# Optimization experiments

Hardware: AMD Instinct MI355X
Metric: run time of the kernel (lower is better)

The kernel has to match this reference:

```python
import jax, jax.numpy as jnp
import numpy as np

SEQ_LEN, BATCH = 200, 4096
VOCAB, EMB_DIM, HID = 50000, 100, 300


def setup_inputs() -> dict:
    key = jax.random.key(0)
    ks = jax.random.split(key, 8)
    s = 0.05  # small init scale to keep tanh unsaturated
    return {
        "x": jax.random.randint(ks[0], (SEQ_LEN, BATCH), 0, VOCAB, dtype=jnp.int64 if jax.config.jax_enable_x64 else jnp.int32),
        "emb": jax.random.normal(ks[1], (VOCAB, EMB_DIM), jnp.float32) * s,
        "W_ih": jax.random.normal(ks[2], (HID, EMB_DIM), jnp.float32) * s,
        "b_ih": jnp.zeros((HID,), jnp.float32),
        "W_hh": jax.random.normal(ks[3], (HID, HID), jnp.float32) * s,
        "b_hh": jnp.zeros((HID,), jnp.float32),
        "W1": jax.random.normal(ks[4], (256, HID), jnp.float32) * s,
        "b1": jnp.zeros((256,), jnp.float32),
        "W2": jax.random.normal(ks[5], (2, 256), jnp.float32) * s,
        "b2": jnp.zeros((2,), jnp.float32),
    }


def reference(x, emb, W_ih, b_ih, W_hh, b_hh, W1, b1, W2, b2):
    # Embedding lookup: [T, B] -> [T, B, E]
    xe = emb[x]
    # Precompute input projections for all timesteps in one big GEMM: [T, B, H]
    xw = jnp.einsum('tbe,he->tbh', xe, W_ih) + b_ih + b_hh
    h0 = jnp.zeros((x.shape[1], W_hh.shape[0]), emb.dtype)

    def step(h, xw_t):
        h = jnp.tanh(xw_t + h @ W_hh.T)  # RNNCell: tanh(x Wih^T + bih + h Whh^T + bhh)
        return h, None

    h, _ = jax.lax.scan(step, h0, xw)
    h = jax.nn.relu(h @ W1.T + b1)
    return h @ W2.T + b2  # [B, 2]
```

## Files before the change

kernel.cpp:

```cpp
#include <hip/hip_runtime.h>

#define SEQ   200
#define BATCH 4096
#define EMB   100
#define HID   300
#define NH1   256
#define BM    16
#define NFRAG 13
#define FRB   14
#define FB    1024
#define BUFB  (FRB * FB)
#define NTMAX 3
#define NHF   10
#define H1P   260
#define PD    10

typedef _Float16 half8 __attribute__((ext_vector_type(8)));
typedef _Float16 half4h __attribute__((ext_vector_type(4)));
typedef float floatx4 __attribute__((ext_vector_type(4)));

__device__ __forceinline__ float fast_tanh(float x) {
    float e = __expf(2.0f * x);
    float r = __builtin_amdgcn_rcpf(e + 1.0f);
    return 1.0f - 2.0f * r;
}

__device__ __forceinline__ int fragoff(int m, int k) {
    return (k >> 5) * FB + ((k >> 3) & 3) * 256 + m * 16 + (k & 7) * 2;
}

#define T_LOOP(NTT)                                                                   \
    _Pragma("unroll 2")                                                               \
    for (int t = 0; t < SEQ; ++t) {                                                   \
        const int p = t & 1;                                                          \
        const char* rb = ub + p * BUFB + rdo;                                         \
        char*       wb = ub + (1 - p) * BUFB;                                         \
        half8 af[NFRAG];                                                              \
        _Pragma("unroll")                                                             \
        for (int kk = 0; kk < PD; ++kk) af[kk] = *(const half8*)(rb + kk * FB);       \
        if (is_st && (t + 1 < SEQ)) {                                                 \
            half4h hv; hv[0] = (_Float16)pf.x; hv[1] = (_Float16)pf.y;                \
                       hv[2] = (_Float16)pf.z; hv[3] = (_Float16)pf.w;                \
            *(half4h*)(wb + xwo) = hv;                                                \
        }                                                                             \
        if (is_st && (t + 2 < SEQ)) {                                                 \
            const int idx = xs[(t + 2) * BM + gr];                                    \
            pf = ((const float4*)emb)[idx * 25 + gc];                                 \
        }                                                                             \
        floatx4 acc[NTT];                                                             \
        _Pragma("unroll")                                                             \
        for (int kk = 0; kk < NFRAG; ++kk) {                                          \
            if (kk + PD < NFRAG) af[kk + PD] = *(const half8*)(rb + (kk + PD) * FB);  \
            _Pragma("unroll")                                                         \
            for (int tt = 0; tt < NTT; ++tt)                                          \
                acc[tt] = __builtin_amdgcn_mfma_f32_16x16x32_f16(                     \
                    Wb[tt][kk], af[kk], (kk == 0) ? biasv[tt] : acc[tt], 0, 0, 0);    \
        }                                                                             \
        _Pragma("unroll")                                                             \
        for (int tt = 0; tt < NTT; ++tt) {                                            \
            half4h hv;                                                                \
            _Pragma("unroll")                                                         \
            for (int r = 0; r < 4; ++r) hv[r] = (_Float16)fast_tanh(acc[tt][r]);      \
            *(half4h*)(wb + hwo[tt]) = hv;                                            \
        }                                                                             \
        asm volatile("s_waitcnt lgkmcnt(0)" ::: "memory");                            \
        __builtin_amdgcn_s_barrier();                                                 \
    }

__global__ void __launch_bounds__(512)
rnn_fused(const int* __restrict__ x, const float* __restrict__ emb,
          const float* __restrict__ W_ih, const float* __restrict__ b_ih,
          const float* __restrict__ W_hh, const float* __restrict__ b_hh,
          const float* __restrict__ W1, const float* __restrict__ b1,
          const float* __restrict__ W2, const float* __restrict__ b2,
          float* __restrict__ out)
{
    __shared__ __align__(16) _Float16 uf[2][FRB][512];
    __shared__ int   xs[SEQ * BM];
    __shared__ float h1s[BM][H1P];

    const int tid  = threadIdx.x;
    const int lane = tid & 63;
    const int w    = tid >> 6;
    const int ln15 = lane & 15;
    const int q    = lane >> 4;
    const int row0 = blockIdx.x * BM;

    const int t0 = (w < 3) ? 3 * w : 2 * w + 3;

    for (int i = tid; i < 2 * FRB * 512 / 2; i += 512) ((unsigned int*)uf)[i] = 0u;
    for (int i = tid; i < SEQ * BM; i += 512)
        xs[i] = x[(size_t)(i >> 4) * BATCH + row0 + (i & 15)];

    half8   Wb[NTMAX][NFRAG];
    floatx4 biasv[NTMAX];
#pragma unroll
    for (int tt = 0; tt < NTMAX; ++tt) {
        const int nb = (t0 + tt) * 16;
#pragma unroll
        for (int r = 0; r < 4; ++r) {
            const int col = nb + 4 * q + r;
            biasv[tt][r] = (col < HID) ? (b_ih[col] + b_hh[col]) : 0.0f;
        }
        const int n = nb + ln15;
#pragma unroll
        for (int kk = 0; kk < NFRAG; ++kk) {
            union { half8 h; unsigned int d[4]; } cv;
#pragma unroll
            for (int j = 0; j < 8; ++j) {
                const int k = kk * 32 + q * 8 + j;
                float v = 0.0f;
                if (n < HID) {
                    if (k < EMB)                        v = W_ih[n * EMB + k];
                    else if (k >= 112 && k < 112 + HID) v = W_hh[n * HID + (k - 112)];
                }
                cv.h[j] = (_Float16)v;
            }
            asm volatile("" : "+v"(cv.d[0]), "+v"(cv.d[1]), "+v"(cv.d[2]), "+v"(cv.d[3]));
            Wb[tt][kk] = cv.h;
        }
    }

    char* ub = (char*)uf;
    const int rdo = lane * 16;
    int hwo[NTMAX];
#pragma unroll
    for (int tt = 0; tt < NTMAX; ++tt)
        hwo[tt] = fragoff(ln15, 112 + (t0 + tt) * 16 + 4 * q);

    const bool is_st = (tid < 400);
    const int  gr = tid / 25, gc = tid - gr * 25;
    const int  xwo = fragoff(gr & 15, gc * 4);
    __syncthreads();

    float4 pf = {0.0f, 0.0f, 0.0f, 0.0f};
    if (is_st) {
        const int idx = xs[gr];
        const float4 f = ((const float4*)emb)[idx * 25 + gc];
        half4h hv; hv[0] = (_Float16)f.x; hv[1] = (_Float16)f.y;
                   hv[2] = (_Float16)f.z; hv[3] = (_Float16)f.w;
        *(half4h*)(ub + xwo) = hv;
        const int idx1 = xs[BM + gr];
        pf = ((const float4*)emb)[idx1 * 25 + gc];
    }
    __syncthreads();

    if (w < 3) {
        T_LOOP(3)
    } else {
        T_LOOP(2)
    }

    {
        const int hro = fragoff(ln15, 112 + q * 8);
        floatx4 hacc[2];
        int ncol[2];
#pragma unroll
        for (int tt = 0; tt < 2; ++tt) {
            const int n = (w * 2 + tt) * 16 + ln15;
            ncol[tt] = n;
            const float b = b1[n];
            hacc[tt][0] = b; hacc[tt][1] = b; hacc[tt][2] = b; hacc[tt][3] = b;
        }
#pragma unroll
        for (int kk = 0; kk < NHF; ++kk) {
            const half8 a = *(const half8*)(ub + hro + kk * FB);
#pragma unroll
            for (int tt = 0; tt < 2; ++tt) {
                half8 bv;
#pragma unroll
                for (int j = 0; j < 8; ++j) {
                    const int k = kk * 32 + q * 8 + j;
                    bv[j] = (_Float16)((k < HID) ? W1[ncol[tt] * HID + k] : 0.0f);
                }
                hacc[tt] = __builtin_amdgcn_mfma_f32_16x16x32_f16(bv, a, hacc[tt], 0, 0, 0);
            }
        }
#pragma unroll
        for (int tt = 0; tt < 2; ++tt) {
            float4 fv;
            fv.x = fmaxf(hacc[tt][0], 0.0f); fv.y = fmaxf(hacc[tt][1], 0.0f);
            fv.z = fmaxf(hacc[tt][2], 0.0f); fv.w = fmaxf(hacc[tt][3], 0.0f);
            *(float4*)&h1s[ln15][(w * 2 + tt) * 16 + 4 * q] = fv;
        }
    }
    __syncthreads();

    if (tid < 32) {
        const int r = tid & 15, o = tid >> 4;
        float a = b2[o];
        const float* ww = W2 + (size_t)o * NH1;
        for (int k = 0; k < NH1; ++k) a += h1s[r][k] * ww[k];
        out[(size_t)(row0 + r) * 2 + o] = a;
    }
}

extern "C" void kernel_launch(void* const* d_in, const int* in_sizes, int n_in,
                              void* d_out, int out_size, void* d_ws, size_t ws_size,
                              hipStream_t stream) {
    const int*   x    = (const int*)d_in[0];
    const float* emb  = (const float*)d_in[1];
    const float* W_ih = (const float*)d_in[2];
    const float* b_ih = (const float*)d_in[3];
    const float* W_hh = (const float*)d_in[4];
    const float* b_hh = (const float*)d_in[5];
    const float* W1   = (const float*)d_in[6];
    const float* b1   = (const float*)d_in[7];
    const float* W2   = (const float*)d_in[8];
    const float* b2   = (const float*)d_in[9];
    float* outp = (float*)d_out;

    hipLaunchKernelGGL(rnn_fused, dim3(BATCH / BM), dim3(512), 0, stream,
                       x, emb, W_ih, b_ih, W_hh, b_hh, W1, b1, W2, b2, outp);
}
```

Before: 326.5 us.

## Halve block to four waves with five output tiles each and redistribute gathers

Shrinks each RNN block from eight waves to four. Each wave now owns five 16-column output tiles of the hidden state (up from two or three), and the embedding-gather work is spread across threads so that some threads load up to three chunks. The aim is to cut per-step barrier cost and the number of waves that must synchronise, and to remove the 3/2 tile imbalance. In exchange, each wave holds more register-resident weight fragments (65 half8), so register pressure and spilling are a risk, and each wave has less latency-hiding parallelism per step.

New measurement: 417.3 us. 1.28x slower.

```diff
diff --git a/kernel.cpp b/kernel.cpp
--- a/kernel.cpp
+++ b/kernel.cpp
@@ -10,10 +10,11 @@
 #define FRB   14
 #define FB    1024
 #define BUFB  (FRB * FB)
-#define NTMAX 3
+#define NTMAX 5
 #define NHF   10
 #define H1P   260
-#define PD    10
+#define PD    7
+#define NCK   3
 
 typedef _Float16 half8 __attribute__((ext_vector_type(8)));
 typedef _Float16 half4h __attribute__((ext_vector_type(4)));
@@ -38,14 +39,20 @@
         half8 af[NFRAG];                                                              \
         _Pragma("unroll")                                                             \
         for (int kk = 0; kk < PD; ++kk) af[kk] = *(const half8*)(rb + kk * FB);       \
-        if (is_st && (t + 1 < SEQ)) {                                                 \
-            half4h hv; hv[0] = (_Float16)pf.x; hv[1] = (_Float16)pf.y;                \
-                       hv[2] = (_Float16)pf.z; hv[3] = (_Float16)pf.w;                \
-            *(half4h*)(wb + xwo) = hv;                                                \
-        }                                                                             \
-        if (is_st && (t + 2 < SEQ)) {                                                 \
-            const int idx = xs[(t + 2) * BM + gr];                                    \
-            pf = ((const float4*)emb)[idx * 25 + gc];                                 \
+        if (t + 1 < SEQ) {                                                            \
+            _Pragma("unroll")                                                         \
+            for (int j = 0; j < NCK; ++j) if (j < nck) {                              \
+                half4h hv; hv[0] = (_Float16)pf[j].x; hv[1] = (_Float16)pf[j].y;      \
+                           hv[2] = (_Float16)pf[j].z; hv[3] = (_Float16)pf[j].w;      \
+                *(half4h*)(wb + xwo[j]) = hv;                                         \
+            }                                                                         \
+        }                                                                             \
+        if (t + 2 < SEQ) {                                                            \
+            _Pragma("unroll")                                                         \
+            for (int j = 0; j < NCK; ++j) if (j < nck) {                              \
+                const int idx = xs[(t + 2) * BM + cgr[j]];                            \
+                pf[j] = ((const float4*)emb)[idx * 25 + cgc[j]];                      \
+            }                                                                         \
         }                                                                             \
         floatx4 acc[NTT];                                                             \
         _Pragma("unroll")                                                             \
@@ -67,7 +74,7 @@
         __builtin_amdgcn_s_barrier();                                                 \
     }
 
-__global__ void __launch_bounds__(512)
+__global__ void __launch_bounds__(256, 1)
 rnn_fused(const int* __restrict__ x, const float* __restrict__ emb,
           const float* __restrict__ W_ih, const float* __restrict__ b_ih,
           const float* __restrict__ W_hh, const float* __restrict__ b_hh,
@@ -86,10 +93,10 @@
     const int q    = lane >> 4;
     const int row0 = blockIdx.x * BM;
 
-    const int t0 = (w < 3) ? 3 * w : 2 * w + 3;
-
-    for (int i = tid; i < 2 * FRB * 512 / 2; i += 512) ((unsigned int*)uf)[i] = 0u;
-    for (int i = tid; i < SEQ * BM; i += 512)
+    const int t0 = 5 * w;
+
+    for (int i = tid; i < 2 * FRB * 512 / 2; i += 256) ((unsigned int*)uf)[i] = 0u;
+    for (int i = tid; i < SEQ * BM; i += 256)
         xs[i] = x[(size_t)(i >> 4) * BATCH + row0 + (i & 15)];
 
     half8   Wb[NTMAX][NFRAG];
@@ -128,36 +135,43 @@
     for (int tt = 0; tt < NTMAX; ++tt)
         hwo[tt] = fragoff(ln15, 112 + (t0 + tt) * 16 + 4 * q);
 
-    const bool is_st = (tid < 400);
-    const int  gr = tid / 25, gc = tid - gr * 25;
-    const int  xwo = fragoff(gr & 15, gc * 4);
+    int nck = 1;
+    int ckid[NCK]; ckid[0] = tid; ckid[1] = 0; ckid[2] = 0;
+    if (tid >= 192)      { ckid[1] = 256 + 2 * (tid - 192); ckid[2] = ckid[1] + 1; nck = 3; }
+    else if (tid >= 176) { ckid[1] = 384 + (tid - 176); nck = 2; }
+    int cgr[NCK], cgc[NCK], xwo[NCK];
+#pragma unroll
+    for (int j = 0; j < NCK; ++j) {
+        const int c = ckid[j];
+        cgr[j] = c / 25; cgc[j] = c - 25 * cgr[j];
+        xwo[j] = fragoff(cgr[j] & 15, cgc[j] * 4);
+    }
     __syncthreads();
 
-    float4 pf = {0.0f, 0.0f, 0.0f, 0.0f};
-    if (is_st) {
-        const int idx = xs[gr];
-        const float4 f = ((const float4*)emb)[idx * 25 + gc];
+    float4 pf[NCK];
+#pragma unroll
+    for (int j = 0; j < NCK; ++j) { pf[j].x = pf[j].y = pf[j].z = pf[j].w = 0.0f; }
+#pragma unroll
+    for (int j = 0; j < NCK; ++j) if (j < nck) {
+        const int idx = xs[cgr[j]];
+        const float4 f = ((const float4*)emb)[idx * 25 + cgc[j]];
         half4h hv; hv[0] = (_Float16)f.x; hv[1] = (_Float16)f.y;
                    hv[2] = (_Float16)f.z; hv[3] = (_Float16)f.w;
-        *(half4h*)(ub + xwo) = hv;
-        const int idx1 = xs[BM + gr];
-        pf = ((const float4*)emb)[idx1 * 25 + gc];
+        *(half4h*)(ub + xwo[j]) = hv;
+        const int idx1 = xs[BM + cgr[j]];
+        pf[j] = ((const float4*)emb)[idx1 * 25 + cgc[j]];
     }
     __syncthreads();
 
-    if (w < 3) {
-        T_LOOP(3)
-    } else {
-        T_LOOP(2)
-    }
+    T_LOOP(5)
 
     {
         const int hro = fragoff(ln15, 112 + q * 8);
-        floatx4 hacc[2];
-        int ncol[2];
-#pragma unroll
-        for (int tt = 0; tt < 2; ++tt) {
-            const int n = (w * 2 + tt) * 16 + ln15;
+        floatx4 hacc[4];
+        int ncol[4];
+#pragma unroll
+        for (int tt = 0; tt < 4; ++tt) {
+            const int n = (w * 4 + tt) * 16 + ln15;
             ncol[tt] = n;
             const float b = b1[n];
             hacc[tt][0] = b; hacc[tt][1] = b; hacc[tt][2] = b; hacc[tt][3] = b;
@@ -166,7 +180,7 @@
         for (int kk = 0; kk < NHF; ++kk) {
             const half8 a = *(const half8*)(ub + hro + kk * FB);
 #pragma unroll
-            for (int tt = 0; tt < 2; ++tt) {
+            for (int tt = 0; tt < 4; ++tt) {
                 half8 bv;
 #pragma unroll
                 for (int j = 0; j < 8; ++j) {
@@ -177,11 +191,11 @@
             }
         }
 #pragma unroll
-        for (int tt = 0; tt < 2; ++tt) {
+        for (int tt = 0; tt < 4; ++tt) {
             float4 fv;
             fv.x = fmaxf(hacc[tt][0], 0.0f); fv.y = fmaxf(hacc[tt][1], 0.0f);
             fv.z = fmaxf(hacc[tt][2], 0.0f); fv.w = fmaxf(hacc[tt][3], 0.0f);
-            *(float4*)&h1s[ln15][(w * 2 + tt) * 16 + 4 * q] = fv;
+            *(float4*)&h1s[ln15][(w * 4 + tt) * 16 + 4 * q] = fv;
         }
     }
     __syncthreads();
@@ -210,6 +224,6 @@
     const float* b2   = (const float*)d_in[9];
     float* outp = (float*)d_out;
 
-    hipLaunchKernelGGL(rnn_fused, dim3(BATCH / BM), dim3(512), 0, stream,
+    hipLaunchKernelGGL(rnn_fused, dim3(BATCH / BM), dim3(256), 0, stream,
                        x, emb, W_ih, b_ih, W_hh, b_hh, W1, b1, W2, b2, outp);
 }
```

## Split input and hidden projections, precompute next step's input MFMA off critical path

Applied to the files above, without the earlier changes.

Separates the fused [x|h] operand buffer into a double-buffered hidden buffer and a triple-buffered embedding buffer. The input projection for step t+1 (4 K-fragments) is now computed after the tanh of step t, so only the 10 hidden-state fragments sit on the serial recurrence path instead of 13. The embedding prefetch distance is extended by one step, and the store-thread mapping is changed to a simpler tid&15 / tid>>4 layout. This adds extra accumulator registers (accn) and LDS, and uses more VGPRs alongside the register-resident weights, which may raise spill or occupancy pressure.

New measurement: 431.9 us. 1.32x slower.

```diff
diff --git a/kernel.cpp b/kernel.cpp
--- a/kernel.cpp
+++ b/kernel.cpp
@@ -6,14 +6,14 @@
 #define HID   300
 #define NH1   256
 #define BM    16
-#define NFRAG 13
-#define FRB   14
+#define NHFR  10
+#define NXFR  4
 #define FB    1024
-#define BUFB  (FRB * FB)
+#define HBUF  (NHFR * FB)
+#define XBUF  (NXFR * FB)
 #define NTMAX 3
 #define NHF   10
 #define H1P   260
-#define PD    10
 
 typedef _Float16 half8 __attribute__((ext_vector_type(8)));
 typedef _Float16 half4h __attribute__((ext_vector_type(4)));
@@ -33,36 +33,55 @@
     _Pragma("unroll 2")                                                               \
     for (int t = 0; t < SEQ; ++t) {                                                   \
         const int p = t & 1;                                                          \
-        const char* rb = ub + p * BUFB + rdo;                                         \
-        char*       wb = ub + (1 - p) * BUFB;                                         \
-        half8 af[NFRAG];                                                              \
-        _Pragma("unroll")                                                             \
-        for (int kk = 0; kk < PD; ++kk) af[kk] = *(const half8*)(rb + kk * FB);       \
-        if (is_st && (t + 1 < SEQ)) {                                                 \
+        const char* rbh = ubh + p * HBUF + rdo;                                       \
+        char*       wbh = ubh + (1 - p) * HBUF;                                       \
+        half8 afh[NHFR];                                                              \
+        _Pragma("unroll")                                                             \
+        for (int kk = 0; kk < NHFR; ++kk) afh[kk] = *(const half8*)(rbh + kk * FB);   \
+        if (is_st && (t + 2 < SEQ)) {                                                 \
             half4h hv; hv[0] = (_Float16)pf.x; hv[1] = (_Float16)pf.y;                \
                        hv[2] = (_Float16)pf.z; hv[3] = (_Float16)pf.w;                \
-            *(half4h*)(wb + xwo) = hv;                                                \
-        }                                                                             \
-        if (is_st && (t + 2 < SEQ)) {                                                 \
-            const int idx = xs[(t + 2) * BM + gr];                                    \
+            *(half4h*)(ubx + sw + xwo) = hv;                                          \
+        }                                                                             \
+        if (is_st && (t + 3 < SEQ)) {                                                 \
+            const int idx = xs[(t + 3) * BM + gr];                                    \
             pf = ((const float4*)emb)[idx * 25 + gc];                                 \
         }                                                                             \
         floatx4 acc[NTT];                                                             \
         _Pragma("unroll")                                                             \
-        for (int kk = 0; kk < NFRAG; ++kk) {                                          \
-            if (kk + PD < NFRAG) af[kk + PD] = *(const half8*)(rb + (kk + PD) * FB);  \
+        for (int tt = 0; tt < NTT; ++tt) acc[tt] = accn[tt];                          \
+        _Pragma("unroll")                                                             \
+        for (int kk = 0; kk < NHFR; ++kk) {                                           \
             _Pragma("unroll")                                                         \
             for (int tt = 0; tt < NTT; ++tt)                                          \
-                acc[tt] = __builtin_amdgcn_mfma_f32_16x16x32_f16(                     \
-                    Wb[tt][kk], af[kk], (kk == 0) ? biasv[tt] : acc[tt], 0, 0, 0);    \
+                acc[tt] = __builtin_amdgcn_mfma_f32_16x16x32_f16(Wh[tt][kk], afh[kk], \
+                                                                 acc[tt], 0, 0, 0);   \
+        }                                                                             \
+        half8 afx[NXFR];                                                              \
+        if (t + 1 < SEQ) {                                                            \
+            _Pragma("unroll")                                                         \
+            for (int kk = 0; kk < NXFR; ++kk)                                         \
+                afx[kk] = *(const half8*)(ubx + sr + rdo + kk * FB);                  \
         }                                                                             \
         _Pragma("unroll")                                                             \
         for (int tt = 0; tt < NTT; ++tt) {                                            \
             half4h hv;                                                                \
             _Pragma("unroll")                                                         \
             for (int r = 0; r < 4; ++r) hv[r] = (_Float16)fast_tanh(acc[tt][r]);      \
-            *(half4h*)(wb + hwo[tt]) = hv;                                            \
-        }                                                                             \
+            *(half4h*)(wbh + hwo[tt]) = hv;                                           \
+        }                                                                             \
+        if (t + 1 < SEQ) {                                                            \
+            _Pragma("unroll")                                                         \
+            for (int tt = 0; tt < NTT; ++tt) {                                        \
+                accn[tt] = biasv[tt];                                                 \
+                _Pragma("unroll")                                                     \
+                for (int kk = 0; kk < NXFR; ++kk)                                     \
+                    accn[tt] = __builtin_amdgcn_mfma_f32_16x16x32_f16(Wx[tt][kk],     \
+                                                      afx[kk], accn[tt], 0, 0, 0);    \
+            }                                                                         \
+        }                                                                             \
+        sw += XBUF; if (sw >= 3 * XBUF) sw = 0;                                       \
+        sr += XBUF; if (sr >= 3 * XBUF) sr = 0;                                       \
         asm volatile("s_waitcnt lgkmcnt(0)" ::: "memory");                            \
         __builtin_amdgcn_s_barrier();                                                 \
     }
@@ -75,7 +94,8 @@
           const float* __restrict__ W2, const float* __restrict__ b2,
           float* __restrict__ out)
 {
-    __shared__ __align__(16) _Float16 uf[2][FRB][512];
+    __shared__ __align__(16) _Float16 ufh[2][NHFR][512];
+    __shared__ __align__(16) _Float16 ufx[3][NXFR][512];
     __shared__ int   xs[SEQ * BM];
     __shared__ float h1s[BM][H1P];
 
@@ -88,11 +108,13 @@
 
     const int t0 = (w < 3) ? 3 * w : 2 * w + 3;
 
-    for (int i = tid; i < 2 * FRB * 512 / 2; i += 512) ((unsigned int*)uf)[i] = 0u;
+    for (int i = tid; i < 2 * NHFR * 512 / 2; i += 512) ((unsigned int*)ufh)[i] = 0u;
+    for (int i = tid; i < 3 * NXFR * 512 / 2; i += 512) ((unsigned int*)ufx)[i] = 0u;
     for (int i = tid; i < SEQ * BM; i += 512)
         xs[i] = x[(size_t)(i >> 4) * BATCH + row0 + (i & 15)];
 
-    half8   Wb[NTMAX][NFRAG];
+    half8   Wh[NTMAX][NHFR];
+    half8   Wx[NTMAX][NXFR];
     floatx4 biasv[NTMAX];
 #pragma unroll
     for (int tt = 0; tt < NTMAX; ++tt) {
@@ -104,46 +126,79 @@
         }
         const int n = nb + ln15;
 #pragma unroll
-        for (int kk = 0; kk < NFRAG; ++kk) {
+        for (int kk = 0; kk < NHFR; ++kk) {
             union { half8 h; unsigned int d[4]; } cv;
 #pragma unroll
             for (int j = 0; j < 8; ++j) {
                 const int k = kk * 32 + q * 8 + j;
-                float v = 0.0f;
-                if (n < HID) {
-                    if (k < EMB)                        v = W_ih[n * EMB + k];
-                    else if (k >= 112 && k < 112 + HID) v = W_hh[n * HID + (k - 112)];
-                }
-                cv.h[j] = (_Float16)v;
+                cv.h[j] = (_Float16)((n < HID && k < HID) ? W_hh[n * HID + k] : 0.0f);
             }
             asm volatile("" : "+v"(cv.d[0]), "+v"(cv.d[1]), "+v"(cv.d[2]), "+v"(cv.d[3]));
-            Wb[tt][kk] = cv.h;
-        }
-    }
-
-    char* ub = (char*)uf;
+            Wh[tt][kk] = cv.h;
+        }
+#pragma unroll
+        for (int kk = 0; kk < NXFR; ++kk) {
+            union { half8 h; unsigned int d[4]; } cv;
+#pragma unroll
+            for (int j = 0; j < 8; ++j) {
+                const int k = kk * 32 + q * 8 + j;
+                cv.h[j] = (_Float16)((n < HID && k < EMB) ? W_ih[n * EMB + k] : 0.0f);
+            }
+            asm volatile("" : "+v"(cv.d[0]), "+v"(cv.d[1]), "+v"(cv.d[2]), "+v"(cv.d[3]));
+            Wx[tt][kk] = cv.h;
+        }
+    }
+
+    char* ubh = (char*)ufh;
+    char* ubx = (char*)ufx;
     const int rdo = lane * 16;
     int hwo[NTMAX];
 #pragma unroll
     for (int tt = 0; tt < NTMAX; ++tt)
-        hwo[tt] = fragoff(ln15, 112 + (t0 + tt) * 16 + 4 * q);
+        hwo[tt] = fragoff(ln15, (t0 + tt) * 16 + 4 * q);
 
     const bool is_st = (tid < 400);
-    const int  gr = tid / 25, gc = tid - gr * 25;
-    const int  xwo = fragoff(gr & 15, gc * 4);
+    const int  gr = tid & 15, gc = tid >> 4;
+    const int  xwo = fragoff(gr, gc * 4);
     __syncthreads();
 
     float4 pf = {0.0f, 0.0f, 0.0f, 0.0f};
     if (is_st) {
-        const int idx = xs[gr];
-        const float4 f = ((const float4*)emb)[idx * 25 + gc];
-        half4h hv; hv[0] = (_Float16)f.x; hv[1] = (_Float16)f.y;
-                   hv[2] = (_Float16)f.z; hv[3] = (_Float16)f.w;
-        *(half4h*)(ub + xwo) = hv;
-        const int idx1 = xs[BM + gr];
-        pf = ((const float4*)emb)[idx1 * 25 + gc];
+        const int i0 = xs[gr];
+        const float4 f0 = ((const float4*)emb)[i0 * 25 + gc];
+        half4h h0; h0[0] = (_Float16)f0.x; h0[1] = (_Float16)f0.y;
+                   h0[2] = (_Float16)f0.z; h0[3] = (_Float16)f0.w;
+        *(half4h*)(ubx + xwo) = h0;
+        const int i1 = xs[BM + gr];
+        const float4 f1 = ((const float4*)emb)[i1 * 25 + gc];
+        half4h h1v; h1v[0] = (_Float16)f1.x; h1v[1] = (_Float16)f1.y;
+                    h1v[2] = (_Float16)f1.z; h1v[3] = (_Float16)f1.w;
+        *(half4h*)(ubx + XBUF + xwo) = h1v;
     }
     __syncthreads();
+
+    floatx4 accn[NTMAX];
+    {
+        half8 afx0[NXFR];
+#pragma unroll
+        for (int kk = 0; kk < NXFR; ++kk)
+            afx0[kk] = *(const half8*)(ubx + rdo + kk * FB);
+#pragma unroll
+        for (int tt = 0; tt < NTMAX; ++tt) {
+            accn[tt] = biasv[tt];
+#pragma unroll
+            for (int kk = 0; kk < NXFR; ++kk)
+                accn[tt] = __builtin_amdgcn_mfma_f32_16x16x32_f16(Wx[tt][kk], afx0[kk],
+                                                                  accn[tt], 0, 0, 0);
+        }
+    }
+    if (is_st) {
+        const int i2 = xs[2 * BM + gr];
+        pf = ((const float4*)emb)[i2 * 25 + gc];
+    }
+
+    int sw = 2 * XBUF;
+    int sr = XBUF;
 
     if (w < 3) {
         T_LOOP(3)
@@ -152,7 +207,7 @@
     }
 
     {
-        const int hro = fragoff(ln15, 112 + q * 8);
+        const int hro = fragoff(ln15, q * 8);
         floatx4 hacc[2];
         int ncol[2];
 #pragma unroll
@@ -164,7 +219,7 @@
         }
 #pragma unroll
         for (int kk = 0; kk < NHF; ++kk) {
-            const half8 a = *(const half8*)(ub + hro + kk * FB);
+            const half8 a = *(const half8*)(ubh + hro + kk * FB);
 #pragma unroll
             for (int tt = 0; tt < 2; ++tt) {
                 half8 bv;
```

## Spread recurrent tiles over twelve waves and restripe embedding prefetch

Applied to the files above, without the earlier changes.

The block grows from 8 to 12 waves, so each wave owns at most 2 output tiles of the hidden state instead of 3. This shortens the serial MFMA chain per timestep, and the fragment prefetch depth is cut to save registers. Embedding prefetch moves to the last 320 threads, with 80 of them loading a second chunk, and only the first 8 waves run the MLP head. The cost is more waves contending for the per-step barrier, plus higher register pressure and lower occupancy limits from the 768-thread launch bound.

New measurement: 336.2 us. 3.0% more time.

```diff
diff --git a/kernel.cpp b/kernel.cpp
--- a/kernel.cpp
+++ b/kernel.cpp
@@ -10,14 +10,14 @@
 #define FRB   14
 #define FB    1024
 #define BUFB  (FRB * FB)
-#define NTMAX 3
+#define NTMAX 2
 #define NHF   10
 #define H1P   260
-#define PD    10
-
-typedef _Float16 half8 __attribute__((ext_vector_type(8)));
+#define PD    4
+
+typedef _Float16 half8  __attribute__((ext_vector_type(8)));
 typedef _Float16 half4h __attribute__((ext_vector_type(4)));
-typedef float floatx4 __attribute__((ext_vector_type(4)));
+typedef float    floatx4 __attribute__((ext_vector_type(4)));
 
 __device__ __forceinline__ float fast_tanh(float x) {
     float e = __expf(2.0f * x);
@@ -39,13 +39,22 @@
         _Pragma("unroll")                                                             \
         for (int kk = 0; kk < PD; ++kk) af[kk] = *(const half8*)(rb + kk * FB);       \
         if (is_st && (t + 1 < SEQ)) {                                                 \
-            half4h hv; hv[0] = (_Float16)pf.x; hv[1] = (_Float16)pf.y;                \
-                       hv[2] = (_Float16)pf.z; hv[3] = (_Float16)pf.w;                \
-            *(half4h*)(wb + xwo) = hv;                                                \
+            half4h hv; hv[0] = (_Float16)pf1.x; hv[1] = (_Float16)pf1.y;              \
+                       hv[2] = (_Float16)pf1.z; hv[3] = (_Float16)pf1.w;              \
+            *(half4h*)(wb + xwo1) = hv;                                               \
+            if (has2) {                                                               \
+                half4h h2; h2[0] = (_Float16)pf2.x; h2[1] = (_Float16)pf2.y;          \
+                           h2[2] = (_Float16)pf2.z; h2[3] = (_Float16)pf2.w;          \
+                *(half4h*)(wb + xwo2) = h2;                                           \
+            }                                                                         \
         }                                                                             \
         if (is_st && (t + 2 < SEQ)) {                                                 \
-            const int idx = xs[(t + 2) * BM + gr];                                    \
-            pf = ((const float4*)emb)[idx * 25 + gc];                                 \
+            const int idx = xs[(t + 2) * BM + gr1];                                   \
+            pf1 = ((const float4*)emb)[idx * 25 + gc1];                               \
+            if (has2) {                                                               \
+                const int idx2 = xs[(t + 2) * BM + gr2];                              \
+                pf2 = ((const float4*)emb)[idx2 * 25 + gc2];                          \
+            }                                                                         \
         }                                                                             \
         floatx4 acc[NTT];                                                             \
         _Pragma("unroll")                                                             \
@@ -67,7 +76,7 @@
         __builtin_amdgcn_s_barrier();                                                 \
     }
 
-__global__ void __launch_bounds__(512)
+__global__ void __launch_bounds__(768)
 rnn_fused(const int* __restrict__ x, const float* __restrict__ emb,
           const float* __restrict__ W_ih, const float* __restrict__ b_ih,
           const float* __restrict__ W_hh, const float* __restrict__ b_hh,
@@ -86,10 +95,10 @@
     const int q    = lane >> 4;
     const int row0 = blockIdx.x * BM;
 
-    const int t0 = (w < 3) ? 3 * w : 2 * w + 3;
-
-    for (int i = tid; i < 2 * FRB * 512 / 2; i += 512) ((unsigned int*)uf)[i] = 0u;
-    for (int i = tid; i < SEQ * BM; i += 512)
+    const int t0 = (w < 7) ? 2 * w : w + 7;
+
+    for (int i = tid; i < 2 * FRB * 512 / 2; i += 768) ((unsigned int*)uf)[i] = 0u;
+    for (int i = tid; i < SEQ * BM; i += 768)
         xs[i] = x[(size_t)(i >> 4) * BATCH + row0 + (i & 15)];
 
     half8   Wb[NTMAX][NFRAG];
@@ -128,30 +137,43 @@
     for (int tt = 0; tt < NTMAX; ++tt)
         hwo[tt] = fragoff(ln15, 112 + (t0 + tt) * 16 + 4 * q);
 
-    const bool is_st = (tid < 400);
-    const int  gr = tid / 25, gc = tid - gr * 25;
-    const int  xwo = fragoff(gr & 15, gc * 4);
+    const bool is_st = (tid >= 448);
+    const int  c1   = tid - 448;
+    const bool has2 = is_st && (c1 < 80);
+    const int  c2   = 320 + c1;
+    const int  gr1 = c1 & 15, gc1 = c1 >> 4;
+    const int  gr2 = c2 & 15, gc2 = c2 >> 4;
+    const int  xwo1 = fragoff(gr1, gc1 * 4);
+    const int  xwo2 = fragoff(gr2, gc2 * 4);
     __syncthreads();
 
-    float4 pf = {0.0f, 0.0f, 0.0f, 0.0f};
+    float4 pf1 = {0.0f, 0.0f, 0.0f, 0.0f};
+    float4 pf2 = {0.0f, 0.0f, 0.0f, 0.0f};
     if (is_st) {
-        const int idx = xs[gr];
-        const float4 f = ((const float4*)emb)[idx * 25 + gc];
-        half4h hv; hv[0] = (_Float16)f.x; hv[1] = (_Float16)f.y;
-                   hv[2] = (_Float16)f.z; hv[3] = (_Float16)f.w;
-        *(half4h*)(ub + xwo) = hv;
-        const int idx1 = xs[BM + gr];
-        pf = ((const float4*)emb)[idx1 * 25 + gc];
+        const int i0 = xs[gr1];
+        const float4 f0 = ((const float4*)emb)[i0 * 25 + gc1];
+        half4h h0; h0[0] = (_Float16)f0.x; h0[1] = (_Float16)f0.y;
+                   h0[2] = (_Float16)f0.z; h0[3] = (_Float16)f0.w;
+        *(half4h*)(ub + xwo1) = h0;
+        if (has2) {
+            const int i02 = xs[gr2];
+            const float4 f02 = ((const float4*)emb)[i02 * 25 + gc2];
+            half4h h2; h2[0] = (_Float16)f02.x; h2[1] = (_Float16)f02.y;
+                       h2[2] = (_Float16)f02.z; h2[3] = (_Float16)f02.w;
+            *(half4h*)(ub + xwo2) = h2;
+        }
+        pf1 = ((const float4*)emb)[xs[BM + gr1] * 25 + gc1];
+        if (has2) pf2 = ((const float4*)emb)[xs[BM + gr2] * 25 + gc2];
     }
     __syncthreads();
 
-    if (w < 3) {
-        T_LOOP(3)
+    if (w < 7) {
+        T_LOOP(2)
     } else {
-        T_LOOP(2)
-    }
-
-    {
+        T_LOOP(1)
+    }
+
+    if (w < 8) {
         const int hro = fragoff(ln15, 112 + q * 8);
         floatx4 hacc[2];
         int ncol[2];
@@ -210,6 +232,6 @@
     const float* b2   = (const float*)d_in[9];
     float* outp = (float*)d_out;
 
-    hipLaunchKernelGGL(rnn_fused, dim3(BATCH / BM), dim3(512), 0, stream,
+    hipLaunchKernelGGL(rnn_fused, dim3(BATCH / BM), dim3(768), 0, stream,
                        x, emb, W_ih, b_ih, W_hh, b_hh, W1, b1, W2, b2, outp);
 }
```
